# Optimization experiments

Measured on AMD Instinct MI355X. Metric: run time of the kernel, lower is better.

## Reference

```python
import jax, jax.numpy as jnp
import numpy as np
from jax import lax

DN = ('NHWC', 'HWIO', 'NHWC')
COMMIT = 0.25  # commitment_cost


def _conv(x, w, b, s):
    return lax.conv_general_dilated(x, w, (s, s), 'SAME', dimension_numbers=DN) + b


def _convT(x, w, b, s):
    return lax.conv_transpose(x, w, (s, s), 'SAME', dimension_numbers=DN) + b


def setup_inputs() -> dict:
    key = jax.random.key(0)
    ks = jax.random.split(key, 12)
    B, H, W = 128, 128, 128
    D, K = 64, 512  # embedding_dim, num_embeddings

    def wp(k, shape):
        fan_in = shape[0] * shape[1] * shape[2]
        return (jax.random.normal(k, shape, jnp.float32) / np.sqrt(fan_in)).astype(jnp.float32)

    return {
        'x': jax.random.uniform(ks[0], (B, H, W, 3), jnp.float32),
        'enc_w1': wp(ks[1], (4, 4, 3, 32)),   'enc_b1': jnp.zeros((32,), jnp.float32),
        'enc_w2': wp(ks[2], (4, 4, 32, 64)),  'enc_b2': jnp.zeros((64,), jnp.float32),
        'enc_w3': wp(ks[3], (4, 4, 64, 128)), 'enc_b3': jnp.zeros((128,), jnp.float32),
        'enc_w4': wp(ks[4], (2, 2, 128, D)),  'enc_b4': jnp.zeros((D,), jnp.float32),
        'emb': jax.random.normal(ks[5], (K, D), jnp.float32),
        'dec_w1': wp(ks[6], (2, 2, D, 128)),  'dec_b1': jnp.zeros((128,), jnp.float32),
        'dec_w2': wp(ks[7], (4, 4, 128, 64)), 'dec_b2': jnp.zeros((64,), jnp.float32),
        'dec_w3': wp(ks[8], (4, 4, 64, 32)),  'dec_b3': jnp.zeros((32,), jnp.float32),
        'dec_w4': wp(ks[9], (4, 4, 32, 3)),   'dec_b4': jnp.zeros((3,), jnp.float32),
    }


def _forward(x, enc_w1, enc_b1, enc_w2, enc_b2, enc_w3, enc_b3, enc_w4, enc_b4,
             emb, dec_w1, dec_b1, dec_w2, dec_b2, dec_w3, dec_b3, dec_w4, dec_b4):
    # ---- encoder: 128 -> 64 -> 32 -> 16 (SAME, stride 2) -> 16 (stride 1) ----
    z = jax.nn.relu(_conv(x, enc_w1, enc_b1, 2))
    z = jax.nn.relu(_conv(z, enc_w2, enc_b2, 2))
    z = jax.nn.relu(_conv(z, enc_w3, enc_b3, 2))
    z = _conv(z, enc_w4, enc_b4, 1)                     # [B, 16, 16, D]

    # ---- vector quantizer ----
    B, D = z.shape[0], emb.shape[1]
    flat = z.reshape(B, -1, D)                          # [B, N, D]
    d2 = (jnp.sum(flat * flat, axis=2, keepdims=True)
          - 2.0 * jnp.einsum('bnd,kd->bnk', flat, emb)
          + jnp.sum(emb * emb, axis=1))                 # [B, N, K]
    idx = jnp.argmin(d2, axis=2)                        # [B, N] int
    q = emb[idx].reshape(z.shape)                       # gather == one_hot @ emb
    loss = COMMIT * jnp.mean((lax.stop_gradient(q) - z) ** 2)
    q_st = z + lax.stop_gradient(q - z)                 # straight-through

    # ---- decoder: 16 -> 16 (stride 1) -> 32 -> 64 -> 128 ----
    y = jax.nn.relu(_convT(q_st, dec_w1, dec_b1, 1))
    y = jax.nn.relu(_convT(y, dec_w2, dec_b2, 2))
    y = jax.nn.relu(_convT(y, dec_w3, dec_b3, 2))
    y = jax.nn.sigmoid(_convT(y, dec_w4, dec_b4, 2))    # [B, 128, 128, 3]
    return y, loss, idx


def reference(x, enc_w1, enc_b1, enc_w2, enc_b2, enc_w3, enc_b3, enc_w4, enc_b4,
              emb, dec_w1, dec_b1, dec_w2, dec_b2, dec_w3, dec_b3, dec_w4, dec_b4):
    return _forward(x, enc_w1, enc_b1, enc_w2, enc_b2, enc_w3, enc_b3, enc_w4, enc_b4,
                    emb, dec_w1, dec_b1, dec_w2, dec_b2, dec_w3, dec_b3, dec_w4, dec_b4)
```

## Files before the change

### kernel.cpp

```cpp
#include <hip/hip_runtime.h>
#include <hip/hip_bf16.h>

typedef __bf16 bf16x8_t __attribute__((ext_vector_type(8)));
typedef float  f32x4_t  __attribute__((ext_vector_type(4)));

__device__ inline bf16x8_t ld_bf16x8(const __hip_bfloat16* p) {
    return *reinterpret_cast<const bf16x8_t*>(p);
}
__device__ inline bf16x8_t zero_bf16x8() {
    bf16x8_t z;
#pragma unroll
    for (int i = 0; i < 8; ++i) z[i] = (__bf16)0.0f;
    return z;
}

__device__ inline void split3f(float v, __bf16& h, __bf16& m, __bf16& l) {
    unsigned u;  __builtin_memcpy(&u, &v, 4);
    unsigned uh = u & 0xffff0000u;
    float fh;    __builtin_memcpy(&fh, &uh, 4);
    float r = v - fh;
    unsigned ur; __builtin_memcpy(&ur, &r, 4);
    unsigned um = ur & 0xffff0000u;
    float fm;    __builtin_memcpy(&fm, &um, 4);
    float r2 = r - fm;
    unsigned ul; __builtin_memcpy(&ul, &r2, 4);
    unsigned short hs = (unsigned short)(uh >> 16);
    unsigned short ms = (unsigned short)(um >> 16);
    unsigned short ls = (unsigned short)(ul >> 16);
    __builtin_memcpy(&h, &hs, 2);
    __builtin_memcpy(&m, &ms, 2);
    __builtin_memcpy(&l, &ls, 2);
}

__global__ __launch_bounds__(256) void enc1_kernel(
    const float* __restrict__ x, const float* __restrict__ w,
    const float* __restrict__ bias, float* __restrict__ y)
{
    __shared__ float xs[34*66*3];
    __shared__ float wsm[1536];

    const int n  = blockIdx.x >> 3;
    const int th = (blockIdx.x >> 1) & 3;
    const int tw = blockIdx.x & 1;
    const int HO0 = th*16, WO0 = tw*32;
    const int HI0 = 2*HO0 - 1, WI0 = 2*WO0 - 1;
    const int t = threadIdx.x;

    for (int i = t; i < 1536; i += 256) wsm[i] = w[i];
    for (int i = t; i < 34*66*3; i += 256) {
        int row = i / 198; int j = i - row*198;
        int wi_l = j / 3;  int c = j - wi_l*3;
        int hi = HI0 + row, wi = WI0 + wi_l;
        float v = 0.0f;
        if (hi >= 0 && hi < 128 && wi >= 0 && wi < 128)
            v = x[((n*128 + hi)*128 + wi)*3 + c];
        xs[i] = v;
    }
    __syncthreads();

    const int wl = t & 15, hl = t >> 4;
    float acc0[32], acc1[32];
#pragma unroll
    for (int f4 = 0; f4 < 8; ++f4) {
        float4 bv = *(const float4*)(bias + 4*f4);
        acc0[4*f4+0]=bv.x; acc0[4*f4+1]=bv.y; acc0[4*f4+2]=bv.z; acc0[4*f4+3]=bv.w;
        acc1[4*f4+0]=bv.x; acc1[4*f4+1]=bv.y; acc1[4*f4+2]=bv.z; acc1[4*f4+3]=bv.w;
    }
    for (int r = 0; r < 4; ++r) {
#pragma unroll
        for (int s = 0; s < 4; ++s) {
#pragma unroll
            for (int c = 0; c < 3; ++c) {
                float xv0 = xs[(2*hl + r)*198 + (2*wl + s)*3 + c];
                float xv1 = xs[(2*hl + r)*198 + (2*(wl+16) + s)*3 + c];
                const float* wp = wsm + ((r*4 + s)*3 + c)*32;
#pragma unroll
                for (int f4 = 0; f4 < 8; ++f4) {
                    float4 wv = *(const float4*)(wp + 4*f4);
                    acc0[4*f4+0] = fmaf(xv0, wv.x, acc0[4*f4+0]);
                    acc0[4*f4+1] = fmaf(xv0, wv.y, acc0[4*f4+1]);
                    acc0[4*f4+2] = fmaf(xv0, wv.z, acc0[4*f4+2]);
                    acc0[4*f4+3] = fmaf(xv0, wv.w, acc0[4*f4+3]);
                    acc1[4*f4+0] = fmaf(xv1, wv.x, acc1[4*f4+0]);
                    acc1[4*f4+1] = fmaf(xv1, wv.y, acc1[4*f4+1]);
                    acc1[4*f4+2] = fmaf(xv1, wv.z, acc1[4*f4+2]);
                    acc1[4*f4+3] = fmaf(xv1, wv.w, acc1[4*f4+3]);
                }
            }
        }
    }
    float* y0 = y + ((size_t)((n*64 + HO0 + hl)*64) + WO0 + wl)*32;
#pragma unroll
    for (int f4 = 0; f4 < 8; ++f4) {
        float4 o0 = make_float4(fmaxf(acc0[4*f4+0],0.f), fmaxf(acc0[4*f4+1],0.f),
                                fmaxf(acc0[4*f4+2],0.f), fmaxf(acc0[4*f4+3],0.f));
        *(float4*)(y0 + 4*f4) = o0;
    }
    float* y1 = y0 + 16*32;
#pragma unroll
    for (int f4 = 0; f4 < 8; ++f4) {
        float4 o1 = make_float4(fmaxf(acc1[4*f4+0],0.f), fmaxf(acc1[4*f4+1],0.f),
                                fmaxf(acc1[4*f4+2],0.f), fmaxf(acc1[4*f4+3],0.f));
        *(float4*)(y1 + 4*f4) = o1;
    }
}

__global__ void prep_wpk(const float* __restrict__ w, __hip_bfloat16* __restrict__ out,
                         int TAPS, int CIN, int COUT)
{
    const int NF = COUT >> 4, KC = CIN >> 5;
    int total = TAPS*3*NF*KC*512;
    int i = blockIdx.x*256 + threadIdx.x;
    if (i >= total) return;
    int tmp = i;
    int j = tmp & 7;      tmp >>= 3;
    int lane = tmp & 63;  tmp >>= 6;
    int kc = tmp % KC;    tmp /= KC;
    int nf = tmp % NF;    tmp /= NF;
    int plane = tmp % 3;  int tap = tmp / 3;
    int l15 = lane & 15, quad = lane >> 4;
    int f = nf*16 + l15;
    int c = kc*32 + quad*8 + j;
    float v = w[(tap*CIN + c)*COUT + f];
    __bf16 h, m, l;
    split3f(v, h, m, l);
    ((__bf16*)out)[i] = (plane == 0) ? h : (plane == 1) ? m : l;
}

__global__ void prep_wdk(const float* __restrict__ w, __hip_bfloat16* __restrict__ out,
                         int TAPS, int CIN, int COUT)
{
    const int NF = COUT >> 4, KC = CIN >> 5;
    int total = TAPS*NF*KC*512;
    int i = blockIdx.x*256 + threadIdx.x;
    if (i >= total) return;
    int tmp = i;
    int j = tmp & 7;      tmp >>= 3;
    int lane = tmp & 63;  tmp >>= 6;
    int kc = tmp % KC;    tmp /= KC;
    int nf = tmp % NF;    tmp /= NF;
    int tap = tmp;
    int l15 = lane & 15, quad = lane >> 4;
    int f = nf*16 + l15;
    int c = kc*32 + quad*8 + j;
    out[i] = __float2bfloat16(w[(tap*CIN + c)*COUT + f]);
}

__global__ void prep_wb4(const float* __restrict__ w, __hip_bfloat16* __restrict__ out)
{
    int i = blockIdx.x*256 + threadIdx.x;
    if (i >= 16*64*8) return;
    int j = i & 7;
    int lane = (i >> 3) & 63;
    int g = i >> 9;
    int f = lane & 15;
    int c = (lane >> 4)*8 + j;
    float v = (f < 3) ? w[g*96 + c*3 + f] : 0.0f;
    out[i] = __float2bfloat16(v);
}

template<int R,int S,int CIN,int COUT,int IWL,int OWL,int STR,int PAD,int ACT,int INF32,int OUTF32,int NSPLIT>
__global__ __launch_bounds__(256) void mfma_encB(
    const void* __restrict__ xin,
    const __hip_bfloat16* __restrict__ wpk,
    const float* __restrict__ bias,
    __hip_bfloat16* __restrict__ yout,
    float* __restrict__ yf)
{
    constexpr int IW = 1 << IWL, OW = 1 << OWL;
    constexpr int NF = COUT / 16, KC = CIN / 32, TAPS = R*S;
    constexpr int NFB = NF / NSPLIT;
    constexpr int PIECE = NFB*KC*64;
    constexpr int CHUNK8 = 3*PIECE;
    __shared__ bf16x8_t ldsB[CHUNK8];

    const int nf0 = (int)blockIdx.y * NFB;
    const int t = threadIdx.x;
    const int wave = t >> 6, lane = t & 63;
    const int l15 = lane & 15, quad = lane >> 4;

    const int m  = blockIdx.x*64 + wave*16 + l15;
    const int wp_ = m & (OW-1);
    const int hp_ = (m >> OWL) & (OW-1);
    const int np_ = m >> (2*OWL);

    f32x4_t acc[NFB];
#pragma unroll
    for (int nf = 0; nf < NFB; ++nf) {
        float bv = bias[(nf0 + nf)*16 + l15];
        acc[nf][0] = bv; acc[nf][1] = bv; acc[nf][2] = bv; acc[nf][3] = bv;
    }
    const bf16x8_t zv = zero_bf16x8();

    for (int tap = 0; tap < TAPS; ++tap) {
        __syncthreads();
        {
            const bf16x8_t* base = (const bf16x8_t*)wpk + (size_t)tap*(3*NF*KC*64);
            for (int i8 = t; i8 < CHUNK8; i8 += 256) {
                int plane = i8 / PIECE;
                int rem = i8 - plane*PIECE;
                ldsB[i8] = base[(size_t)(plane*NF + nf0)*KC*64 + rem];
            }
        }
        __syncthreads();

        const int r = tap / S, s = tap % S;
        const int hi = hp_*STR - PAD + r;
        const int wi = wp_*STR - PAD + s;
        const bool v = (hi >= 0) && (hi < IW) && (wi >= 0) && (wi < IW);
        const int hic = v ? hi : 0, wic = v ? wi : 0;
        const size_t pix = (size_t)(np_*IW + hic)*IW + wic;

#pragma unroll
        for (int kc = 0; kc < KC; ++kc) {
            bf16x8_t ah, am_, al_;
            if (INF32) {
                const float* af = (const float*)xin + pix*CIN + kc*32 + quad*8;
                float xv[8];
                if (v) {
                    *(float4*)(xv+0) = *(const float4*)(af);
                    *(float4*)(xv+4) = *(const float4*)(af + 4);
                } else {
#pragma unroll
                    for (int jj = 0; jj < 8; ++jj) xv[jj] = 0.0f;
                }
#pragma unroll
                for (int jj = 0; jj < 8; ++jj) {
                    __bf16 th, tm, tl;
                    split3f(xv[jj], th, tm, tl);
                    ah[jj] = th; am_[jj] = tm; al_[jj] = tl;
                }
            } else {
                const __hip_bfloat16* ap = (const __hip_bfloat16*)xin
                    + pix*(3*CIN) + kc*32 + quad*8;
                ah  = v ? ld_bf16x8(ap)           : zv;
                am_ = v ? ld_bf16x8(ap + CIN)     : zv;
                al_ = v ? ld_bf16x8(ap + 2*CIN)   : zv;
            }
#pragma unroll
            for (int nf = 0; nf < NFB; ++nf) {
                bf16x8_t bh = ldsB[(0*NFB + nf)*KC*64 + kc*64 + lane];
                bf16x8_t bm = ldsB[(1*NFB + nf)*KC*64 + kc*64 + lane];
                bf16x8_t bl = ldsB[(2*NFB + nf)*KC*64 + kc*64 + lane];
                acc[nf] = __builtin_amdgcn_mfma_f32_16x16x32_bf16(al_, bh, acc[nf], 0, 0, 0);
                acc[nf] = __builtin_amdgcn_mfma_f32_16x16x32_bf16(ah,  bl, acc[nf], 0, 0, 0);
                acc[nf] = __builtin_amdgcn_mfma_f32_16x16x32_bf16(am_, bm, acc[nf], 0, 0, 0);
                acc[nf] = __builtin_amdgcn_mfma_f32_16x16x32_bf16(am_, bh, acc[nf], 0, 0, 0);
                acc[nf] = __builtin_amdgcn_mfma_f32_16x16x32_bf16(ah,  bm, acc[nf], 0, 0, 0);
                acc[nf] = __builtin_amdgcn_mfma_f32_16x16x32_bf16(ah,  bh, acc[nf], 0, 0, 0);
            }
        }
    }

#pragma unroll
    for (int nf = 0; nf < NFB; ++nf) {
#pragma unroll
        for (int i = 0; i < 4; ++i) {
            int mo = blockIdx.x*64 + wave*16 + quad*4 + i;
            int wo = mo & (OW-1), ho = (mo >> OWL) & (OW-1), no = mo >> (2*OWL);
            size_t opix = (size_t)(no*OW + ho)*OW + wo;
            float vv = acc[nf][i];
            if (ACT) vv = fmaxf(vv, 0.0f);
            if (OUTF32) {
                yf[opix*COUT + (nf0 + nf)*16 + l15] = vv;
            } else {
                __bf16 h, mm2, l;
                split3f(vv, h, mm2, l);
                __bf16* yb = (__bf16*)yout + opix*(3*COUT) + (nf0 + nf)*16 + l15;
                yb[0]        = h;
                yb[COUT]     = mm2;
                yb[2*COUT]   = l;
            }
        }
    }
}

template<int CIN,int COUT,int SWL,int CONVT,int NSPLIT>
__global__ __launch_bounds__(256) void mfma_decB(
    const __hip_bfloat16* __restrict__ xin,
    const __hip_bfloat16* __restrict__ wdk,
    const float* __restrict__ bias,
    __hip_bfloat16* __restrict__ yout)
{
    constexpr int SW = 1 << SWL;
    constexpr int NF = COUT / 16, KC = CIN / 32;
    constexpr int NFB = NF / NSPLIT;
    constexpr int CHUNK8 = NFB*KC*64;
    __shared__ bf16x8_t ldsB[CHUNK8];

    const int ph = CONVT ? (int)(blockIdx.y >> 1) : 0;
    const int pw = CONVT ? (int)(blockIdx.y & 1) : 0;
    const int nf0 = (CONVT ? (int)blockIdx.z : (int)blockIdx.y) * NFB;
    const int t = threadIdx.x;
    const int wave = t >> 6, lane = t & 63;
    const int l15 = lane & 15, quad = lane >> 4;

    const int m  = blockIdx.x*64 + wave*16 + l15;
    const int wp_ = m & (SW-1);
    const int hp_ = (m >> SWL) & (SW-1);
    const int np_ = m >> (2*SWL);

    f32x4_t acc[NFB];
#pragma unroll
    for (int nf = 0; nf < NFB; ++nf) {
        float bv = bias[(nf0 + nf)*16 + l15];
        acc[nf][0] = bv; acc[nf][1] = bv; acc[nf][2] = bv; acc[nf][3] = bv;
    }
    const bf16x8_t zv = zero_bf16x8();

    for (int tap = 0; tap < 4; ++tap) {
        const int rr = tap >> 1, ss = tap & 1;
        const int widx = CONVT ? ((ph + 2*rr)*4 + (pw + 2*ss)) : tap;
        __syncthreads();
        {
            const bf16x8_t* base = (const bf16x8_t*)wdk
                + (size_t)widx*(NF*KC*64) + (size_t)nf0*KC*64;
            for (int i8 = t; i8 < CHUNK8; i8 += 256) ldsB[i8] = base[i8];
        }
        __syncthreads();

        const int hi = hp_ + ph - 1 + rr;
        const int wi = wp_ + pw - 1 + ss;
        const bool v = (hi >= 0) && (hi < SW) && (wi >= 0) && (wi < SW);
        const int hic = v ? hi : 0, wic = v ? wi : 0;
        const __hip_bfloat16* ap = xin + (size_t)((np_*SW + hic)*SW + wic)*CIN + quad*8;
#pragma unroll
        for (int kc = 0; kc < KC; ++kc) {
            bf16x8_t a = v ? ld_bf16x8(ap + kc*32) : zv;
#pragma unroll
            for (int nf = 0; nf < NFB; ++nf) {
                bf16x8_t b = ldsB[(nf*KC + kc)*64 + lane];
                acc[nf] = __builtin_amdgcn_mfma_f32_16x16x32_bf16(a, b, acc[nf], 0, 0, 0);
            }
        }
    }

    constexpr int HOUT = CONVT ? 2*SW : SW;
#pragma unroll
    for (int nf = 0; nf < NFB; ++nf) {
#pragma unroll
        for (int i = 0; i < 4; ++i) {
            int mo = blockIdx.x*64 + wave*16 + quad*4 + i;
            int wo = mo & (SW-1), ho = (mo >> SWL) & (SW-1), no = mo >> (2*SWL);
            int hoo = CONVT ? 2*ho + ph : ho;
            int woo = CONVT ? 2*wo + pw : wo;
            float vv = fmaxf(acc[nf][i], 0.0f);
            yout[((size_t)(no*HOUT + hoo)*HOUT + woo)*COUT + (nf0 + nf)*16 + l15] = __float2bfloat16(vv);
        }
    }
}

__global__ __launch_bounds__(256) void dec4_mfma(
    const __hip_bfloat16* __restrict__ x, const __hip_bfloat16* __restrict__ wb,
    const float* __restrict__ bias, float* __restrict__ y)
{
    __shared__ __hip_bfloat16 xs[6*66*40];

    const int n  = blockIdx.x >> 4;
    const int R0 = (blockIdx.x & 15) * 4;
    const int t  = threadIdx.x;
    const int wave = t >> 6, lane = t & 63;
    const int l15 = lane & 15, quad = lane >> 4;

    bf16x8_t wreg[16];
#pragma unroll
    for (int g = 0; g < 16; ++g)
        wreg[g] = ld_bf16x8(wb + (size_t)(g*64 + lane)*8);

    const float bv = (l15 < 3) ? bias[l15] : 0.0f;

    for (int slot = t; slot < 6*66*4; slot += 256) {
        int row = slot / 264;
        int rem = slot - row*264;
        int col = rem >> 2, c8 = rem & 3;
        int xi = R0 - 1 + row, xc = col - 1;
        uint4 val = make_uint4(0u,0u,0u,0u);
        if (xi >= 0 && xi < 64 && xc >= 0 && xc < 64)
            val = *(const uint4*)(x + ((size_t)((n*64 + xi)*64) + xc)*32 + c8*8);
        *(uint4*)(xs + (row*66 + col)*40 + c8*8) = val;
    }
    __syncthreads();

    for (int r4 = 0; r4 < 4; ++r4) {
        bf16x8_t af[3][3];
#pragma unroll
        for (int dr = 0; dr < 3; ++dr)
#pragma unroll
            for (int dc = 0; dc < 3; ++dc)
                af[dr][dc] = *(const bf16x8_t*)(xs
                    + ((r4 + dr)*66 + (wave*16 + l15 + dc))*40 + quad*8);

#pragma unroll
        for (int ph = 0; ph < 2; ++ph)
#pragma unroll
        for (int pw = 0; pw < 2; ++pw) {
            f32x4_t acc;
            acc[0] = bv; acc[1] = bv; acc[2] = bv; acc[3] = bv;
#pragma unroll
            for (int rr = 0; rr < 2; ++rr)
#pragma unroll
            for (int ss = 0; ss < 2; ++ss) {
                const int g = (ph + 2*rr)*4 + (pw + 2*ss);
                acc = __builtin_amdgcn_mfma_f32_16x16x32_bf16(
                          af[ph+rr][pw+ss], wreg[g], acc, 0, 0, 0);
            }
            if (l15 < 3) {
#pragma unroll
                for (int i = 0; i < 4; ++i) {
                    int pc = wave*16 + quad*4 + i;
                    int ho = 2*(R0 + r4) + ph, wo = 2*pc + pw;
                    float vv = 1.0f / (1.0f + __expf(-acc[i]));
                    y[((size_t)(n*128 + ho)*128 + wo)*3 + l15] = vv;
                }
            }
        }
    }
}

__global__ void zero_loss(float* p) {
    if (threadIdx.x == 0 && blockIdx.x == 0) *p = 0.0f;
}

__global__ __launch_bounds__(256) void vq_kernel(
    const float* __restrict__ z, const float* __restrict__ emb,
    __hip_bfloat16* __restrict__ qb, float* __restrict__ idx_out,
    float* __restrict__ loss_out, float loss_scale)
{
    __shared__ float zs[64*65];
    __shared__ float es[64*64];
    __shared__ float gd[4*64];
    __shared__ int   gi[4*64];
    __shared__ float md[64];
    __shared__ int   mi[64];

    const int t = threadIdx.x;
    const int pos0 = blockIdx.x * 64;

    for (int j = t; j < 64*64; j += 256)
        zs[(j >> 6)*65 + (j & 63)] = z[pos0*64 + j];
    __syncthreads();

    const int pos = t & 63;
    const int grp = t >> 6;
    float zr[64];
#pragma unroll
    for (int d = 0; d < 64; ++d) zr[d] = zs[pos*65 + d];

    float bestd = 3.4e38f;
    int   besti = 0;

    for (int ck = 0; ck < 8; ++ck) {
        __syncthreads();
        for (int j = t; j < 4096; j += 256) es[j] = emb[ck*4096 + j];
        __syncthreads();
#pragma unroll
        for (int k = 0; k < 16; ++k) {
            const int cc = grp + 4*k;
            const float4* ep = (const float4*)(es + cc*64);
            float acc = 0.0f;
#pragma unroll
            for (int u = 0; u < 16; ++u) {
                float4 e = ep[u];
                float d0 = zr[4*u+0] - e.x;
                float d1 = zr[4*u+1] - e.y;
                float d2 = zr[4*u+2] - e.z;
                float d3 = zr[4*u+3] - e.w;
                acc = fmaf(d0,d0,acc); acc = fmaf(d1,d1,acc);
                acc = fmaf(d2,d2,acc); acc = fmaf(d3,d3,acc);
            }
            const int code = ck*64 + cc;
            if (acc < bestd) { bestd = acc; besti = code; }
        }
    }
    gd[grp*64 + pos] = bestd;
    gi[grp*64 + pos] = besti;
    __syncthreads();
    if (grp == 0) {
        float bd = gd[pos]; int bi = gi[pos];
#pragma unroll
        for (int g2 = 1; g2 < 4; ++g2) {
            float dv = gd[g2*64 + pos]; int iv = gi[g2*64 + pos];
            if (dv < bd || (dv == bd && iv < bi)) { bd = dv; bi = iv; }
        }
        md[pos] = bd; mi[pos] = bi;
        idx_out[pos0 + pos] = (float)bi;
    }
    __syncthreads();
    for (int j = t; j < 4096; j += 256) {
        int p = j >> 6, d = j & 63;
        qb[pos0*64 + j] = __float2bfloat16(emb[mi[p]*64 + d]);
    }
    if (t == 0) {
        float s = 0.0f;
        for (int p = 0; p < 64; ++p) s += md[p];
        atomicAdd(loss_out, s * loss_scale);
    }
}

extern "C" void kernel_launch(void* const* d_in, const int* in_sizes, int n_in,
                              void* d_out, int out_size, void* d_ws, size_t ws_size,
                              hipStream_t stream)
{
    const float* x   = (const float*)d_in[0];
    const float* ew1 = (const float*)d_in[1];  const float* eb1 = (const float*)d_in[2];
    const float* ew2 = (const float*)d_in[3];  const float* eb2 = (const float*)d_in[4];
    const float* ew3 = (const float*)d_in[5];  const float* eb3 = (const float*)d_in[6];
    const float* ew4 = (const float*)d_in[7];  const float* eb4 = (const float*)d_in[8];
    const float* emb = (const float*)d_in[9];
    const float* dw1 = (const float*)d_in[10]; const float* db1 = (const float*)d_in[11];
    const float* dw2 = (const float*)d_in[12]; const float* db2 = (const float*)d_in[13];
    const float* dw3 = (const float*)d_in[14]; const float* db3 = (const float*)d_in[15];
    const float* dw4 = (const float*)d_in[16]; const float* db4 = (const float*)d_in[17];

    float* outy = (float*)d_out;
    float* outl = outy + 6291456;
    float* outi = outl + 1;

    char* W = (char*)d_ws;
    float*          e1  = (float*)         (W + 0);
    __hip_bfloat16* e2p = (__hip_bfloat16*)(W + 67108864);
    __hip_bfloat16* e3p = (__hip_bfloat16*)(W + 0);
    float*          z   = (float*)         (W + 25165824);
    __hip_bfloat16* qb  = (__hip_bfloat16*)(W + 33554432);
    __hip_bfloat16* d1o = (__hip_bfloat16*)(W + 37748736);
    __hip_bfloat16* d2o = (__hip_bfloat16*)(W + 46137344);
    __hip_bfloat16* d3o = (__hip_bfloat16*)(W + 67108864);
    __hip_bfloat16* wp2 = (__hip_bfloat16*)(W + 117440512);
    __hip_bfloat16* wp3 = wp2 + 98304;
    __hip_bfloat16* wp4 = wp3 + 393216;
    __hip_bfloat16* wd1 = wp4 + 98304;
    __hip_bfloat16* wd2 = wd1 + 32768;
    __hip_bfloat16* wd3 = wd2 + 131072;
    __hip_bfloat16* wb4 = wd3 + 32768;

    hipLaunchKernelGGL(prep_wpk, dim3(384),  dim3(256), 0, stream, ew2, wp2, 16, 32, 64);
    hipLaunchKernelGGL(prep_wpk, dim3(1536), dim3(256), 0, stream, ew3, wp3, 16, 64, 128);
    hipLaunchKernelGGL(prep_wpk, dim3(384),  dim3(256), 0, stream, ew4, wp4, 4, 128, 64);
    hipLaunchKernelGGL(prep_wdk, dim3(128),  dim3(256), 0, stream, dw1, wd1, 4, 64, 128);
    hipLaunchKernelGGL(prep_wdk, dim3(512),  dim3(256), 0, stream, dw2, wd2, 16, 128, 64);
    hipLaunchKernelGGL(prep_wdk, dim3(128),  dim3(256), 0, stream, dw3, wd3, 16, 64, 32);
    hipLaunchKernelGGL(prep_wb4, dim3(32),   dim3(256), 0, stream, dw4, wb4);

    hipLaunchKernelGGL(enc1_kernel, dim3(1024), dim3(256), 0, stream, x, ew1, eb1, e1);
    hipLaunchKernelGGL((mfma_encB<4,4,32,64,6,5,2,1,1,1,0,1>), dim3(2048), dim3(256), 0, stream,
                       (const void*)e1, wp2, eb2, e2p, (float*)nullptr);
    hipLaunchKernelGGL((mfma_encB<4,4,64,128,5,4,2,1,1,0,0,2>), dim3(512,2), dim3(256), 0, stream,
                       (const void*)e2p, wp3, eb3, e3p, (float*)nullptr);
    hipLaunchKernelGGL((mfma_encB<2,2,128,64,4,4,1,0,0,0,1,2>), dim3(512,2), dim3(256), 0, stream,
                       (const void*)e3p, wp4, eb4, (__hip_bfloat16*)nullptr, z);

    hipLaunchKernelGGL(zero_loss, dim3(1), dim3(64), 0, stream, outl);
    hipLaunchKernelGGL(vq_kernel, dim3(512), dim3(256), 0, stream,
                       z, emb, qb, outi, outl, 0.25f / 2097152.0f);

    hipLaunchKernelGGL((mfma_decB<64,128,4,0,2>), dim3(512,2),  dim3(256), 0, stream, qb,  wd1, db1, d1o);
    hipLaunchKernelGGL((mfma_decB<128,64,4,1,1>), dim3(512,4),  dim3(256), 0, stream, d1o, wd2, db2, d2o);
    hipLaunchKernelGGL((mfma_decB<64,32,5,1,1>),  dim3(2048,4), dim3(256), 0, stream, d2o, wd3, db3, d3o);
    hipLaunchKernelGGL(dec4_mfma, dim3(2048), dim3(256), 0, stream, d3o, wb4, db4, outy);
}
```

Before: 526.9 us.

## Compute VQ distances with split-bf16 MFMA matmul instead of scalar loops

```diff
diff --git a/kernel.cpp b/kernel.cpp
--- a/kernel.cpp
+++ b/kernel.cpp
@@ -159,6 +159,35 @@
     out[i] = __float2bfloat16(v);
 }
 
+__global__ void prep_wek(const float* __restrict__ emb, __hip_bfloat16* __restrict__ out)
+{
+    int i = blockIdx.x*256 + threadIdx.x;
+    if (i >= 32*2*3*512) return;
+    int tmp = i;
+    int j = tmp & 7;      tmp >>= 3;
+    int lane = tmp & 63;  tmp >>= 6;
+    int plane = tmp % 3;  tmp /= 3;
+    int kc = tmp & 1;     int nf = tmp >> 1;
+    int code = nf*16 + (lane & 15);
+    int c = kc*32 + (lane >> 4)*8 + j;
+    float v = emb[code*64 + c];
+    __bf16 h, m, l;
+    split3f(v, h, m, l);
+    ((__bf16*)out)[i] = (plane == 0) ? h : (plane == 1) ? m : l;
+}
+
+__global__ void prep_se(const float* __restrict__ emb, float* __restrict__ se)
+{
+    int k = blockIdx.x*256 + threadIdx.x;
+    if (k >= 512) return;
+    float s = 0.0f;
+    for (int d = 0; d < 64; ++d) {
+        float e = emb[k*64 + d];
+        s = fmaf(e, e, s);
+    }
+    se[k] = s;
+}
+
 template<int R,int S,int CIN,int COUT,int IWL,int OWL,int STR,int PAD,int ACT,int INF32,int OUTF32,int NSPLIT>
 __global__ __launch_bounds__(256) void mfma_encB(
     const void* __restrict__ xin,
@@ -421,80 +450,112 @@
     if (threadIdx.x == 0 && blockIdx.x == 0) *p = 0.0f;
 }
 
-__global__ __launch_bounds__(256) void vq_kernel(
-    const float* __restrict__ z, const float* __restrict__ emb,
+__global__ __launch_bounds__(256) void vq_mfma(
+    const float* __restrict__ z, const __hip_bfloat16* __restrict__ wek,
+    const float* __restrict__ se, const float* __restrict__ emb,
     __hip_bfloat16* __restrict__ qb, float* __restrict__ idx_out,
     float* __restrict__ loss_out, float loss_scale)
 {
-    __shared__ float zs[64*65];
-    __shared__ float es[64*64];
-    __shared__ float gd[4*64];
-    __shared__ int   gi[4*64];
-    __shared__ float md[64];
+    __shared__ float ses[512];
+    __shared__ float rv[64*16];
+    __shared__ int   ri[64*16];
     __shared__ int   mi[64];
+    __shared__ float lred[256];
 
     const int t = threadIdx.x;
+    const int wave = t >> 6, lane = t & 63;
+    const int l15 = lane & 15, quad = lane >> 4;
     const int pos0 = blockIdx.x * 64;
 
-    for (int j = t; j < 64*64; j += 256)
-        zs[(j >> 6)*65 + (j & 63)] = z[pos0*64 + j];
+    for (int i = t; i < 512; i += 256) ses[i] = se[i];
+
+    const int prow = pos0 + wave*16 + l15;
+    bf16x8_t ah[2], am[2], al[2];
+#pragma unroll
+    for (int kc = 0; kc < 2; ++kc) {
+        float xv[8];
+        *(float4*)(xv+0) = *(const float4*)(z + (size_t)prow*64 + kc*32 + quad*8);
+        *(float4*)(xv+4) = *(const float4*)(z + (size_t)prow*64 + kc*32 + quad*8 + 4);
+#pragma unroll
+        for (int jj = 0; jj < 8; ++jj) {
+            __bf16 th, tm, tl;
+            split3f(xv[jj], th, tm, tl);
+            ah[kc][jj] = th; am[kc][jj] = tm; al[kc][jj] = tl;
+        }
+    }
+
+    f32x4_t acc[32];
+#pragma unroll
+    for (int nf = 0; nf < 32; ++nf) {
+        acc[nf][0] = 0.f; acc[nf][1] = 0.f; acc[nf][2] = 0.f; acc[nf][3] = 0.f;
+    }
+
+#pragma unroll 8
+    for (int nf = 0; nf < 32; ++nf) {
+#pragma unroll
+        for (int kc = 0; kc < 2; ++kc) {
+            const bf16x8_t* bp = (const bf16x8_t*)wek + (size_t)((nf*2 + kc)*3)*64 + lane;
+            bf16x8_t bh = bp[0];
+            bf16x8_t bm = bp[64];
+            bf16x8_t bl = bp[128];
+            acc[nf] = __builtin_amdgcn_mfma_f32_16x16x32_bf16(al[kc], bh, acc[nf], 0, 0, 0);
+            acc[nf] = __builtin_amdgcn_mfma_f32_16x16x32_bf16(ah[kc], bl, acc[nf], 0, 0, 0);
+            acc[nf] = __builtin_amdgcn_mfma_f32_16x16x32_bf16(am[kc], bm, acc[nf], 0, 0, 0);
+            acc[nf] = __builtin_amdgcn_mfma_f32_16x16x32_bf16(am[kc], bh, acc[nf], 0, 0, 0);
+            acc[nf] = __builtin_amdgcn_mfma_f32_16x16x32_bf16(ah[kc], bm, acc[nf], 0, 0, 0);
+            acc[nf] = __builtin_amdgcn_mfma_f32_16x16x32_bf16(ah[kc], bh, acc[nf], 0, 0, 0);
+        }
+    }
     __syncthreads();
 
-    const int pos = t & 63;
-    const int grp = t >> 6;
-    float zr[64];
-#pragma unroll
-    for (int d = 0; d < 64; ++d) zr[d] = zs[pos*65 + d];
-
-    float bestd = 3.4e38f;
-    int   besti = 0;
-
-    for (int ck = 0; ck < 8; ++ck) {
-        __syncthreads();
-        for (int j = t; j < 4096; j += 256) es[j] = emb[ck*4096 + j];
-        __syncthreads();
-#pragma unroll
-        for (int k = 0; k < 16; ++k) {
-            const int cc = grp + 4*k;
-            const float4* ep = (const float4*)(es + cc*64);
-            float acc = 0.0f;
-#pragma unroll
-            for (int u = 0; u < 16; ++u) {
-                float4 e = ep[u];
-                float d0 = zr[4*u+0] - e.x;
-                float d1 = zr[4*u+1] - e.y;
-                float d2 = zr[4*u+2] - e.z;
-                float d3 = zr[4*u+3] - e.w;
-                acc = fmaf(d0,d0,acc); acc = fmaf(d1,d1,acc);
-                acc = fmaf(d2,d2,acc); acc = fmaf(d3,d3,acc);
-            }
-            const int code = ck*64 + cc;
-            if (acc < bestd) { bestd = acc; besti = code; }
-        }
-    }
-    gd[grp*64 + pos] = bestd;
-    gi[grp*64 + pos] = besti;
+    float best[4]; int bidx[4];
+#pragma unroll
+    for (int i = 0; i < 4; ++i) { best[i] = 3.4e38f; bidx[i] = 0; }
+#pragma unroll
+    for (int nf = 0; nf < 32; ++nf) {
+        const int code = nf*16 + l15;
+        const float seC = ses[code];
+#pragma unroll
+        for (int i = 0; i < 4; ++i) {
+            float d = fmaf(-2.0f, acc[nf][i], seC);
+            if (d < best[i]) { best[i] = d; bidx[i] = code; }
+        }
+    }
+#pragma unroll
+    for (int i = 0; i < 4; ++i) {
+        int p = wave*16 + quad*4 + i;
+        rv[p*16 + l15] = best[i];
+        ri[p*16 + l15] = bidx[i];
+    }
     __syncthreads();
-    if (grp == 0) {
-        float bd = gd[pos]; int bi = gi[pos];
-#pragma unroll
-        for (int g2 = 1; g2 < 4; ++g2) {
-            float dv = gd[g2*64 + pos]; int iv = gi[g2*64 + pos];
-            if (dv < bd || (dv == bd && iv < bi)) { bd = dv; bi = iv; }
-        }
-        md[pos] = bd; mi[pos] = bi;
-        idx_out[pos0 + pos] = (float)bi;
+    if (t < 64) {
+        float bd = rv[t*16]; int bi = ri[t*16];
+#pragma unroll
+        for (int k = 1; k < 16; ++k) {
+            float v = rv[t*16 + k]; int id = ri[t*16 + k];
+            if (v < bd || (v == bd && id < bi)) { bd = v; bi = id; }
+        }
+        mi[t] = bi;
+        idx_out[pos0 + t] = (float)bi;
     }
     __syncthreads();
+
+    float part = 0.0f;
     for (int j = t; j < 4096; j += 256) {
         int p = j >> 6, d = j & 63;
-        qb[pos0*64 + j] = __float2bfloat16(emb[mi[p]*64 + d]);
-    }
-    if (t == 0) {
-        float s = 0.0f;
-        for (int p = 0; p < 64; ++p) s += md[p];
-        atomicAdd(loss_out, s * loss_scale);
-    }
+        float ev = emb[(size_t)mi[p]*64 + d];
+        float zz = z[(size_t)(pos0 + p)*64 + d];
+        float df = ev - zz;
+        part = fmaf(df, df, part);
+        qb[(size_t)pos0*64 + j] = __float2bfloat16(ev);
+    }
+    lred[t] = part;
+    __syncthreads();
+    for (int s = 128; s > 0; s >>= 1) {
+        if (t < s) lred[t] += lred[t + s];
+        __syncthreads();
+    }
+    if (t == 0) atomicAdd(loss_out, lred[0] * loss_scale);
 }
 
 extern "C" void kernel_launch(void* const* d_in, const int* in_sizes, int n_in,
@@ -532,6 +593,8 @@
     __hip_bfloat16* wd2 = wd1 + 32768;
     __hip_bfloat16* wd3 = wd2 + 131072;
     __hip_bfloat16* wb4 = wd3 + 32768;
+    __hip_bfloat16* wek = wb4 + 8192;
+    float*          seb = (float*)(wek + 98304);
 
     hipLaunchKernelGGL(prep_wpk, dim3(384),  dim3(256), 0, stream, ew2, wp2, 16, 32, 64);
     hipLaunchKernelGGL(prep_wpk, dim3(1536), dim3(256), 0, stream, ew3, wp3, 16, 64, 128);
@@ -540,6 +603,8 @@
     hipLaunchKernelGGL(prep_wdk, dim3(512),  dim3(256), 0, stream, dw2, wd2, 16, 128, 64);
     hipLaunchKernelGGL(prep_wdk, dim3(128),  dim3(256), 0, stream, dw3, wd3, 16, 64, 32);
     hipLaunchKernelGGL(prep_wb4, dim3(32),   dim3(256), 0, stream, dw4, wb4);
+    hipLaunchKernelGGL(prep_wek, dim3(384),  dim3(256), 0, stream, emb, wek);
+    hipLaunchKernelGGL(prep_se,  dim3(2),    dim3(256), 0, stream, emb, seb);
 
     hipLaunchKernelGGL(enc1_kernel, dim3(1024), dim3(256), 0, stream, x, ew1, eb1, e1);
     hipLaunchKernelGGL((mfma_encB<4,4,32,64,6,5,2,1,1,1,0,1>), dim3(2048), dim3(256), 0, stream,
@@ -550,8 +615,8 @@
                        (const void*)e3p, wp4, eb4, (__hip_bfloat16*)nullptr, z);
 
     hipLaunchKernelGGL(zero_loss, dim3(1), dim3(64), 0, stream, outl);
-    hipLaunchKernelGGL(vq_kernel, dim3(512), dim3(256), 0, stream,
-                       z, emb, qb, outi, outl, 0.25f / 2097152.0f);
+    hipLaunchKernelGGL(vq_mfma, dim3(512), dim3(256), 0, stream,
+                       z, wek, seb, emb, qb, outi, outl, 0.25f / 2097152.0f);
 
     hipLaunchKernelGGL((mfma_decB<64,128,4,0,2>), dim3(512,2),  dim3(256), 0, stream, qb,  wd1, db1, d1o);
     hipLaunchKernelGGL((mfma_decB<128,64,4,1,1>), dim3(512,4),  dim3(256), 0, stream, d1o, wd2, db2, d2o);
```

Measured after the change: 535.5 us. Within noise of the previous version (+1.6%).
